# Kernel optimization log

Hardware: AMD Instinct MI355X
Metric: run time of the kernel (lower is better)

The kernel has to match this reference:

```python
import jax, jax.numpy as jnp
import numpy as np

B, S, D, H = 2, 2048, 512, 8
HS = D // H  # head_size = 64


def setup_inputs() -> dict:
    key = jax.random.key(0)
    ks = jax.random.split(key, 6)
    scale = 1.0 / np.sqrt(D)
    return {
        "seq_input": jax.random.normal(ks[0], (B, S, D), dtype=jnp.float32),
        "w_X": jax.random.uniform(ks[1], (B, S, S), dtype=jnp.float32),
        "mask": jax.random.uniform(ks[2], (B, S), dtype=jnp.float32),
        "wq": jax.random.normal(ks[3], (D, D), dtype=jnp.float32) * scale,
        "bq": jnp.zeros((D,), dtype=jnp.float32),
        "wk": jax.random.normal(ks[4], (D, D), dtype=jnp.float32) * scale,
        "bk": jnp.zeros((D,), dtype=jnp.float32),
        "wv": jax.random.normal(ks[5], (D, D), dtype=jnp.float32) * scale,
        "bv": jnp.zeros((D,), dtype=jnp.float32),
    }


def reference(seq_input, w_X, mask, wq, bq, wk, bk, wv, bv):
    b, s, d = seq_input.shape
    # Linear projections, split into heads: [b, h, s, hs]
    def proj(w, bias):
        y = jnp.einsum("bsd,ed->bse", seq_input, w) + bias
        return y.reshape(b, s, H, HS).transpose(0, 2, 1, 3)

    Q = proj(wq, bq)
    K = proj(wk, bk)
    V = proj(wv, bv)

    sim = jnp.einsum("bhqe,bhke->bhqk", Q, K) / np.sqrt(HS).astype(np.float32)
    sim = jax.nn.softmax(sim, axis=3)
    # post-softmax multiplicative edge weights, broadcast over heads
    sim = sim * w_X[:, None, :, :]
    # mask zeroes query rows (torch permute trick broadcasts mask over key dim)
    sim = sim * mask[:, None, :, None]

    new_V = jnp.einsum("bhqk,bhke->bhqe", sim, V)  # [b, h, s, hs]
    return new_V.transpose(0, 2, 1, 3).reshape(b, s, d)
```

## Files before the change

kernel.cpp:

```cpp
#include <hip/hip_runtime.h>

#define NB 2
#define NS 2048
#define ND 512
#define NH 8
#define NHS 64

typedef __attribute__((ext_vector_type(4))) float f32x4;
typedef __attribute__((ext_vector_type(8))) short s16x8;

__device__ inline unsigned short f2bf(float f) {
  unsigned int u = __float_as_uint(f);
  unsigned int r = (u + 0x7FFFu + ((u >> 16) & 1u)) >> 16;
  return (unsigned short)r;
}
__device__ inline int swz(int row, int col) { return row * 64 + (col ^ ((row & 7) << 3)); }

__device__ inline s16x8 pack8(const f32x4& a0, const f32x4& a1) {
  s16x8 v;
#pragma unroll
  for (int j = 0; j < 4; ++j) { v[j] = (short)f2bf(a0[j]); v[4 + j] = (short)f2bf(a1[j]); }
  return v;
}

__global__ __launch_bounds__(256) void kv_kernel(
    const float* __restrict__ X, const float* __restrict__ wk, const float* __restrict__ wv,
    const float* __restrict__ bk, const float* __restrict__ bv,
    unsigned short* __restrict__ Kb, unsigned short* __restrict__ Vt) {
  __shared__ __align__(16) unsigned short As[64 * 64];
  __shared__ __align__(16) unsigned short Bs[128 * 64];
  const int tid = threadIdx.x;
  const int lane = tid & 63, wid = tid >> 6;
  const int lr = lane & 15, lh = lane >> 4;
  const int m0 = blockIdx.y * 64;
  const int nb = blockIdx.x;
  const int type = nb >> 2;
  const int wrow0 = (nb & 3) * 128;
  const float* W = (type == 0) ? wk : wv;
  const float* bias = (type == 0) ? bk : bv;
  const int wm = wid >> 1, wn = wid & 1;

  f32x4 acc[2][4] = {};
  f32x4 ar[2][2], br[4][2];

#define KV_LOAD(K0)                                                          \
  {                                                                          \
    _Pragma("unroll") for (int g = 0; g < 2; ++g) {                          \
      int idx = tid + 256 * g; int row = idx >> 3, c8 = (idx & 7) * 8;       \
      const float* pa = X + (size_t)(m0 + row) * 512 + (K0) + c8;            \
      ar[g][0] = *(const f32x4*)pa; ar[g][1] = *(const f32x4*)(pa + 4);      \
    }                                                                        \
    _Pragma("unroll") for (int g = 0; g < 4; ++g) {                          \
      int idx = tid + 256 * g; int row = idx >> 3, c8 = (idx & 7) * 8;       \
      const float* pb = W + (size_t)(wrow0 + row) * 512 + (K0) + c8;         \
      br[g][0] = *(const f32x4*)pb; br[g][1] = *(const f32x4*)(pb + 4);      \
    }                                                                        \
  }

  KV_LOAD(0);
  for (int k0 = 0; k0 < 512; k0 += 64) {
#pragma unroll
    for (int g = 0; g < 2; ++g) {
      int idx = tid + 256 * g; int row = idx >> 3, c8 = (idx & 7) * 8;
      *(s16x8*)&As[swz(row, c8)] = pack8(ar[g][0], ar[g][1]);
    }
#pragma unroll
    for (int g = 0; g < 4; ++g) {
      int idx = tid + 256 * g; int row = idx >> 3, c8 = (idx & 7) * 8;
      *(s16x8*)&Bs[swz(row, c8)] = pack8(br[g][0], br[g][1]);
    }
    __syncthreads();
    if (k0 < 448) KV_LOAD(k0 + 64);
#pragma unroll
    for (int kk = 0; kk < 64; kk += 32) {
      s16x8 af[2], bf_[4];
#pragma unroll
      for (int f = 0; f < 2; ++f) af[f] = *(const s16x8*)&As[swz(wm * 32 + f * 16 + lr, kk + lh * 8)];
#pragma unroll
      for (int f = 0; f < 4; ++f) bf_[f] = *(const s16x8*)&Bs[swz(wn * 64 + f * 16 + lr, kk + lh * 8)];
#pragma unroll
      for (int fm = 0; fm < 2; ++fm)
#pragma unroll
        for (int fn = 0; fn < 4; ++fn)
          acc[fm][fn] = __builtin_amdgcn_mfma_f32_16x16x32_bf16(af[fm], bf_[fn], acc[fm][fn], 0, 0, 0);
    }
    __syncthreads();
  }
#undef KV_LOAD

#pragma unroll
  for (int fn = 0; fn < 4; ++fn) {
    int n = wrow0 + wn * 64 + fn * 16 + lr;
    int hh = n >> 6, hs = n & 63;
    float bb = bias[n];
#pragma unroll
    for (int fm = 0; fm < 2; ++fm) {
#pragma unroll
      for (int r = 0; r < 4; ++r) {
        int m = m0 + wm * 32 + fm * 16 + lh * 4 + r;
        int b = m >> 11, s = m & 2047;
        float val = acc[fm][fn][r] + bb;
        if (type == 0) {
          Kb[((size_t)(b * 8 + hh) * 2048 + s) * 64 + hs] = f2bf(val);
        } else {
          Vt[((size_t)(b * 8 + hh) * 64 + hs) * 2048 + s] = f2bf(val);
        }
      }
    }
  }
}

__global__ __launch_bounds__(256) void attn_kernel(
    const float* __restrict__ X, const float* __restrict__ wq, const float* __restrict__ bq,
    const unsigned short* __restrict__ Kb, const unsigned short* __restrict__ Vt,
    const float* __restrict__ wX, const float* __restrict__ mask, float* __restrict__ out) {
  __shared__ __align__(16) unsigned short Ks[64 * 64];
  __shared__ __align__(16) unsigned short Vs[64 * 64];
  __shared__ __align__(16) unsigned short Qs[64 * 64];
  __shared__ __align__(16) unsigned short Ps[4 * 16 * 64];
  const int tid = threadIdx.x;
  const int lane = tid & 63, wid = tid >> 6;
  const int lr = lane & 15, lh = lane >> 4;
  const int qt = blockIdx.x, hh = blockIdx.y, b = blockIdx.z;
  const int bh = b * 8 + hh;
  const int q0 = qt * 64;

  const int srow = tid >> 3, sc8 = (tid & 7) * 8;
  const int srow1 = (tid + 256) >> 3;

  f32x4 qacc[4] = {};
  f32x4 xr[2][2], wr0[2][2];
#define Q_LOAD(K0)                                                           \
  {                                                                          \
    _Pragma("unroll") for (int g = 0; g < 2; ++g) {                          \
      int row = g ? srow1 : srow;                                            \
      const float* px = X + (size_t)(b * 2048 + q0 + row) * 512 + (K0) + sc8;\
      const float* pw = wq + (size_t)(hh * 64 + row) * 512 + (K0) + sc8;     \
      xr[g][0] = *(const f32x4*)px; xr[g][1] = *(const f32x4*)(px + 4);      \
      wr0[g][0] = *(const f32x4*)pw; wr0[g][1] = *(const f32x4*)(pw + 4);    \
    }                                                                        \
  }
  Q_LOAD(0);
  for (int k0 = 0; k0 < 512; k0 += 64) {
#pragma unroll
    for (int g = 0; g < 2; ++g) {
      int row = g ? srow1 : srow;
      *(s16x8*)&Ks[swz(row, sc8)] = pack8(xr[g][0], xr[g][1]);
      *(s16x8*)&Vs[swz(row, sc8)] = pack8(wr0[g][0], wr0[g][1]);
    }
    __syncthreads();
    if (k0 < 448) Q_LOAD(k0 + 64);
#pragma unroll
    for (int kk = 0; kk < 64; kk += 32) {
      s16x8 xa = *(const s16x8*)&Ks[swz(wid * 16 + lr, kk + lh * 8)];
#pragma unroll
      for (int fn = 0; fn < 4; ++fn) {
        s16x8 wf = *(const s16x8*)&Vs[swz(fn * 16 + lr, kk + lh * 8)];
        qacc[fn] = __builtin_amdgcn_mfma_f32_16x16x32_bf16(xa, wf, qacc[fn], 0, 0, 0);
      }
    }
    __syncthreads();
  }
#undef Q_LOAD

  const int qrow_base = q0 + wid * 16 + lh * 4;
  const float* wxp = wX + ((size_t)b * 2048 + qrow_base) * 2048;

  s16x8 kreg[2], vreg[2];
  float wxf[4][4];
#define KV_TILE_LOAD(KT)                                                     \
  {                                                                          \
    _Pragma("unroll") for (int g = 0; g < 2; ++g) {                          \
      int row = g ? srow1 : srow;                                            \
      kreg[g] = *(const s16x8*)(Kb + ((size_t)bh * 2048 + (KT) * 64 + row) * 64 + sc8); \
      vreg[g] = *(const s16x8*)(Vt + ((size_t)bh * 64 + row) * 2048 + (KT) * 64 + sc8); \
    }                                                                        \
  }
#define WX_LOAD(KT)                                                          \
  {                                                                          \
    _Pragma("unroll") for (int f = 0; f < 4; ++f) {                          \
      int key = (KT) * 64 + f * 16 + lr;                                     \
      _Pragma("unroll") for (int r = 0; r < 4; ++r)                          \
        wxf[f][r] = wxp[(size_t)r * 2048 + key];                             \
    }                                                                        \
  }
  KV_TILE_LOAD(0);
  WX_LOAD(0);

#pragma unroll
  for (int fn = 0; fn < 4; ++fn) {
    int col = fn * 16 + lr;
    float bb = bq[hh * 64 + col];
#pragma unroll
    for (int r = 0; r < 4; ++r) {
      int row = wid * 16 + lh * 4 + r;
      Qs[swz(row, col)] = f2bf((qacc[fn][r] + bb) * 0.125f);
    }
  }
  __syncthreads();

  s16x8 qa[2];
#pragma unroll
  for (int c = 0; c < 2; ++c) qa[c] = *(const s16x8*)&Qs[swz(wid * 16 + lr, c * 32 + lh * 8)];

  float m_[4], l_[4];
  f32x4 o[4] = {};
#pragma unroll
  for (int r = 0; r < 4; ++r) { m_[r] = -__builtin_inff(); l_[r] = 0.f; }

  for (int kt = 0; kt < 32; ++kt) {
#pragma unroll
    for (int g = 0; g < 2; ++g) {
      int row = g ? srow1 : srow;
      *(s16x8*)&Ks[swz(row, sc8)] = kreg[g];
      *(s16x8*)&Vs[swz(row, sc8)] = vreg[g];
    }
    __syncthreads();
    if (kt + 1 < 32) KV_TILE_LOAD(kt + 1);

    f32x4 sv[4] = {};
#pragma unroll
    for (int c = 0; c < 2; ++c) {
#pragma unroll
      for (int f = 0; f < 4; ++f) {
        s16x8 kf = *(const s16x8*)&Ks[swz(f * 16 + lr, c * 32 + lh * 8)];
        sv[f] = __builtin_amdgcn_mfma_f32_16x16x32_bf16(qa[c], kf, sv[f], 0, 0, 0);
      }
    }

    float tm[4];
#pragma unroll
    for (int r = 0; r < 4; ++r)
      tm[r] = fmaxf(fmaxf(sv[0][r], sv[1][r]), fmaxf(sv[2][r], sv[3][r]));
#pragma unroll
    for (int off = 1; off < 16; off <<= 1)
#pragma unroll
      for (int r = 0; r < 4; ++r) tm[r] = fmaxf(tm[r], __shfl_xor(tm[r], off));

    float sc[4];
#pragma unroll
    for (int r = 0; r < 4; ++r) {
      float nm = fmaxf(m_[r], tm[r]);
      sc[r] = __expf(m_[r] - nm);
      m_[r] = nm;
      l_[r] *= sc[r];
    }
#pragma unroll
    for (int f = 0; f < 4; ++f)
#pragma unroll
      for (int r = 0; r < 4; ++r) o[f][r] *= sc[r];

    float ls[4] = {0.f, 0.f, 0.f, 0.f};
#pragma unroll
    for (int f = 0; f < 4; ++f) {
#pragma unroll
      for (int r = 0; r < 4; ++r) {
        float p = __expf(sv[f][r] - m_[r]);
        ls[r] += p;
        Ps[wid * 1024 + swz(lh * 4 + r, f * 16 + lr)] = f2bf(p * wxf[f][r]);
      }
    }
    if (kt + 1 < 32) WX_LOAD(kt + 1);
#pragma unroll
    for (int off = 1; off < 16; off <<= 1)
#pragma unroll
      for (int r = 0; r < 4; ++r) ls[r] += __shfl_xor(ls[r], off);
#pragma unroll
    for (int r = 0; r < 4; ++r) l_[r] += ls[r];

#pragma unroll
    for (int c = 0; c < 2; ++c) {
      s16x8 pf = *(const s16x8*)&Ps[wid * 1024 + swz(lr, c * 32 + lh * 8)];
#pragma unroll
      for (int f = 0; f < 4; ++f) {
        s16x8 vf = *(const s16x8*)&Vs[swz(f * 16 + lr, c * 32 + lh * 8)];
        o[f] = __builtin_amdgcn_mfma_f32_16x16x32_bf16(pf, vf, o[f], 0, 0, 0);
      }
    }
    __syncthreads();
  }
#undef KV_TILE_LOAD
#undef WX_LOAD

#pragma unroll
  for (int r = 0; r < 4; ++r) {
    int q = qrow_base + r;
    float mk = mask[b * 2048 + q];
    float inv = mk / l_[r];
#pragma unroll
    for (int f = 0; f < 4; ++f) {
      out[((size_t)(b * 2048 + q)) * 512 + hh * 64 + f * 16 + lr] = o[f][r] * inv;
    }
  }
}

extern "C" void kernel_launch(void* const* d_in, const int* in_sizes, int n_in,
                              void* d_out, int out_size, void* d_ws, size_t ws_size,
                              hipStream_t stream) {
  const float* X = (const float*)d_in[0];
  const float* wX = (const float*)d_in[1];
  const float* mask = (const float*)d_in[2];
  const float* wq = (const float*)d_in[3];
  const float* bq = (const float*)d_in[4];
  const float* wk = (const float*)d_in[5];
  const float* bk = (const float*)d_in[6];
  const float* wv = (const float*)d_in[7];
  const float* bv = (const float*)d_in[8];
  float* out = (float*)d_out;

  unsigned short* Kb = (unsigned short*)d_ws;
  unsigned short* Vt = Kb + 2097152;

  kv_kernel<<<dim3(8, 64), 256, 0, stream>>>(X, wk, wv, bk, bv, Kb, Vt);
  attn_kernel<<<dim3(32, 8, 2), 256, 0, stream>>>(X, wq, bq, Kb, Vt, wX, mask, out);
}
```

Measured before the change: 185.4 us.

## Transpose QK^T MFMA so each lane owns a query row, vectorize w_X loads

The attention kernel now computes S^T (K as the A operand), so each lane holds one query row's scores. Row max and sum reductions then need two cross-lane shuffles instead of four rounds over four rows, and w_X can be read as contiguous float4 vectors instead of strided scalars. P is written to shared memory as packed 8-byte stores. Separately, the KV projection kernel moves to 512 threads with a 2x4 wave layout. Extra __shfl calls redistribute the scale and sum values back to the output layout.

```diff
diff --git a/kernel.cpp b/kernel.cpp
--- a/kernel.cpp
+++ b/kernel.cpp
@@ -1,13 +1,8 @@
 #include <hip/hip_runtime.h>
-
-#define NB 2
-#define NS 2048
-#define ND 512
-#define NH 8
-#define NHS 64
 
 typedef __attribute__((ext_vector_type(4))) float f32x4;
 typedef __attribute__((ext_vector_type(8))) short s16x8;
+typedef __attribute__((ext_vector_type(2))) unsigned int u32x2;
 
 __device__ inline unsigned short f2bf(float f) {
   unsigned int u = __float_as_uint(f);
@@ -23,7 +18,7 @@
   return v;
 }
 
-__global__ __launch_bounds__(256) void kv_kernel(
+__global__ __launch_bounds__(512) void kv_kernel(
     const float* __restrict__ X, const float* __restrict__ wk, const float* __restrict__ wv,
     const float* __restrict__ bk, const float* __restrict__ bv,
     unsigned short* __restrict__ Kb, unsigned short* __restrict__ Vt) {
@@ -38,20 +33,18 @@
   const int wrow0 = (nb & 3) * 128;
   const float* W = (type == 0) ? wk : wv;
   const float* bias = (type == 0) ? bk : bv;
-  const int wm = wid >> 1, wn = wid & 1;
-
-  f32x4 acc[2][4] = {};
-  f32x4 ar[2][2], br[4][2];
+  const int wm = wid >> 2, wn = wid & 3;
+
+  f32x4 acc[2][2] = {};
+  f32x4 ar[2], br[2][2];
 
 #define KV_LOAD(K0)                                                          \
   {                                                                          \
+    { int row = tid >> 3, c8 = (tid & 7) * 8;                                \
+      const float* pa = X + (size_t)(m0 + row) * 512 + (K0) + c8;            \
+      ar[0] = *(const f32x4*)pa; ar[1] = *(const f32x4*)(pa + 4); }          \
     _Pragma("unroll") for (int g = 0; g < 2; ++g) {                          \
-      int idx = tid + 256 * g; int row = idx >> 3, c8 = (idx & 7) * 8;       \
-      const float* pa = X + (size_t)(m0 + row) * 512 + (K0) + c8;            \
-      ar[g][0] = *(const f32x4*)pa; ar[g][1] = *(const f32x4*)(pa + 4);      \
-    }                                                                        \
-    _Pragma("unroll") for (int g = 0; g < 4; ++g) {                          \
-      int idx = tid + 256 * g; int row = idx >> 3, c8 = (idx & 7) * 8;       \
+      int idx = tid + 512 * g; int row = idx >> 3, c8 = (idx & 7) * 8;       \
       const float* pb = W + (size_t)(wrow0 + row) * 512 + (K0) + c8;         \
       br[g][0] = *(const f32x4*)pb; br[g][1] = *(const f32x4*)(pb + 4);      \
     }                                                                        \
@@ -59,29 +52,28 @@
 
   KV_LOAD(0);
   for (int k0 = 0; k0 < 512; k0 += 64) {
+    {
+      int row = tid >> 3, c8 = (tid & 7) * 8;
+      *(s16x8*)&As[swz(row, c8)] = pack8(ar[0], ar[1]);
+    }
 #pragma unroll
     for (int g = 0; g < 2; ++g) {
-      int idx = tid + 256 * g; int row = idx >> 3, c8 = (idx & 7) * 8;
-      *(s16x8*)&As[swz(row, c8)] = pack8(ar[g][0], ar[g][1]);
-    }
-#pragma unroll
-    for (int g = 0; g < 4; ++g) {
-      int idx = tid + 256 * g; int row = idx >> 3, c8 = (idx & 7) * 8;
+      int idx = tid + 512 * g; int row = idx >> 3, c8 = (idx & 7) * 8;
       *(s16x8*)&Bs[swz(row, c8)] = pack8(br[g][0], br[g][1]);
     }
     __syncthreads();
     if (k0 < 448) KV_LOAD(k0 + 64);
 #pragma unroll
     for (int kk = 0; kk < 64; kk += 32) {
-      s16x8 af[2], bf_[4];
+      s16x8 af[2], bf_[2];
 #pragma unroll
       for (int f = 0; f < 2; ++f) af[f] = *(const s16x8*)&As[swz(wm * 32 + f * 16 + lr, kk + lh * 8)];
 #pragma unroll
-      for (int f = 0; f < 4; ++f) bf_[f] = *(const s16x8*)&Bs[swz(wn * 64 + f * 16 + lr, kk + lh * 8)];
+      for (int f = 0; f < 2; ++f) bf_[f] = *(const s16x8*)&Bs[swz(wn * 32 + f * 16 + lr, kk + lh * 8)];
 #pragma unroll
       for (int fm = 0; fm < 2; ++fm)
 #pragma unroll
-        for (int fn = 0; fn < 4; ++fn)
+        for (int fn = 0; fn < 2; ++fn)
           acc[fm][fn] = __builtin_amdgcn_mfma_f32_16x16x32_bf16(af[fm], bf_[fn], acc[fm][fn], 0, 0, 0);
     }
     __syncthreads();
@@ -89,8 +81,8 @@
 #undef KV_LOAD
 
 #pragma unroll
-  for (int fn = 0; fn < 4; ++fn) {
-    int n = wrow0 + wn * 64 + fn * 16 + lr;
+  for (int fn = 0; fn < 2; ++fn) {
+    int n = wrow0 + wn * 32 + fn * 16 + lr;
     int hh = n >> 6, hs = n & 63;
     float bb = bias[n];
 #pragma unroll
@@ -164,10 +156,11 @@
 #undef Q_LOAD
 
   const int qrow_base = q0 + wid * 16 + lh * 4;
-  const float* wxp = wX + ((size_t)b * 2048 + qrow_base) * 2048;
+  const int q_sm = q0 + wid * 16 + lr;
+  const float* wxq = wX + ((size_t)b * 2048 + q_sm) * 2048;
 
   s16x8 kreg[2], vreg[2];
-  float wxf[4][4];
+  f32x4 wxv[4];
 #define KV_TILE_LOAD(KT)                                                     \
   {                                                                          \
     _Pragma("unroll") for (int g = 0; g < 2; ++g) {                          \
@@ -178,11 +171,8 @@
   }
 #define WX_LOAD(KT)                                                          \
   {                                                                          \
-    _Pragma("unroll") for (int f = 0; f < 4; ++f) {                          \
-      int key = (KT) * 64 + f * 16 + lr;                                     \
-      _Pragma("unroll") for (int r = 0; r < 4; ++r)                          \
-        wxf[f][r] = wxp[(size_t)r * 2048 + key];                             \
-    }                                                                        \
+    _Pragma("unroll") for (int f = 0; f < 4; ++f)                            \
+      wxv[f] = *(const f32x4*)(wxq + (KT) * 64 + f * 16 + lh * 4);           \
   }
   KV_TILE_LOAD(0);
   WX_LOAD(0);
@@ -203,10 +193,8 @@
 #pragma unroll
   for (int c = 0; c < 2; ++c) qa[c] = *(const s16x8*)&Qs[swz(wid * 16 + lr, c * 32 + lh * 8)];
 
-  float m_[4], l_[4];
+  float m_ = -__builtin_inff(), l_ = 0.f;
   f32x4 o[4] = {};
-#pragma unroll
-  for (int r = 0; r < 4; ++r) { m_[r] = -__builtin_inff(); l_[r] = 0.f; }
 
   for (int kt = 0; kt < 32; ++kt) {
 #pragma unroll
@@ -224,49 +212,49 @@
 #pragma unroll
       for (int f = 0; f < 4; ++f) {
         s16x8 kf = *(const s16x8*)&Ks[swz(f * 16 + lr, c * 32 + lh * 8)];
-        sv[f] = __builtin_amdgcn_mfma_f32_16x16x32_bf16(qa[c], kf, sv[f], 0, 0, 0);
-      }
-    }
-
-    float tm[4];
-#pragma unroll
-    for (int r = 0; r < 4; ++r)
-      tm[r] = fmaxf(fmaxf(sv[0][r], sv[1][r]), fmaxf(sv[2][r], sv[3][r]));
-#pragma unroll
-    for (int off = 1; off < 16; off <<= 1)
-#pragma unroll
-      for (int r = 0; r < 4; ++r) tm[r] = fmaxf(tm[r], __shfl_xor(tm[r], off));
-
-    float sc[4];
-#pragma unroll
-    for (int r = 0; r < 4; ++r) {
-      float nm = fmaxf(m_[r], tm[r]);
-      sc[r] = __expf(m_[r] - nm);
-      m_[r] = nm;
-      l_[r] *= sc[r];
-    }
+        sv[f] = __builtin_amdgcn_mfma_f32_16x16x32_bf16(kf, qa[c], sv[f], 0, 0, 0);
+      }
+    }
+
+    float t0 = fmaxf(fmaxf(sv[0][0], sv[0][1]), fmaxf(sv[0][2], sv[0][3]));
+    float t1 = fmaxf(fmaxf(sv[1][0], sv[1][1]), fmaxf(sv[1][2], sv[1][3]));
+    float t2 = fmaxf(fmaxf(sv[2][0], sv[2][1]), fmaxf(sv[2][2], sv[2][3]));
+    float t3 = fmaxf(fmaxf(sv[3][0], sv[3][1]), fmaxf(sv[3][2], sv[3][3]));
+    float tm = fmaxf(fmaxf(t0, t1), fmaxf(t2, t3));
+    tm = fmaxf(tm, __shfl_xor(tm, 16));
+    tm = fmaxf(tm, __shfl_xor(tm, 32));
+
+    float nm = fmaxf(m_, tm);
+    float sc = __expf(m_ - nm);
+    m_ = nm;
+    l_ *= sc;
+    float sc_o[4];
+#pragma unroll
+    for (int r = 0; r < 4; ++r) sc_o[r] = __shfl(sc, 20 * lh + r);
 #pragma unroll
     for (int f = 0; f < 4; ++f)
 #pragma unroll
-      for (int r = 0; r < 4; ++r) o[f][r] *= sc[r];
-
-    float ls[4] = {0.f, 0.f, 0.f, 0.f};
+      for (int r = 0; r < 4; ++r) o[f][r] *= sc_o[r];
+
+    float ls = 0.f;
 #pragma unroll
     for (int f = 0; f < 4; ++f) {
+      float pw[4];
 #pragma unroll
       for (int r = 0; r < 4; ++r) {
-        float p = __expf(sv[f][r] - m_[r]);
-        ls[r] += p;
-        Ps[wid * 1024 + swz(lh * 4 + r, f * 16 + lr)] = f2bf(p * wxf[f][r]);
-      }
+        float p = __expf(sv[f][r] - m_);
+        ls += p;
+        pw[r] = p * wxv[f][r];
+      }
+      u32x2 pk;
+      pk[0] = (unsigned int)f2bf(pw[0]) | ((unsigned int)f2bf(pw[1]) << 16);
+      pk[1] = (unsigned int)f2bf(pw[2]) | ((unsigned int)f2bf(pw[3]) << 16);
+      *(u32x2*)&Ps[wid * 1024 + swz(lr, f * 16 + lh * 4)] = pk;
     }
     if (kt + 1 < 32) WX_LOAD(kt + 1);
-#pragma unroll
-    for (int off = 1; off < 16; off <<= 1)
-#pragma unroll
-      for (int r = 0; r < 4; ++r) ls[r] += __shfl_xor(ls[r], off);
-#pragma unroll
-    for (int r = 0; r < 4; ++r) l_[r] += ls[r];
+    ls += __shfl_xor(ls, 16);
+    ls += __shfl_xor(ls, 32);
+    l_ += ls;
 
 #pragma unroll
     for (int c = 0; c < 2; ++c) {
@@ -282,11 +270,14 @@
 #undef KV_TILE_LOAD
 #undef WX_LOAD
 
+  float l_o[4];
+#pragma unroll
+  for (int r = 0; r < 4; ++r) l_o[r] = __shfl(l_, 20 * lh + r);
 #pragma unroll
   for (int r = 0; r < 4; ++r) {
     int q = qrow_base + r;
     float mk = mask[b * 2048 + q];
-    float inv = mk / l_[r];
+    float inv = mk / l_o[r];
 #pragma unroll
     for (int f = 0; f < 4; ++f) {
       out[((size_t)(b * 2048 + q)) * 512 + hh * 64 + f * 16 + lr] = o[f][r] * inv;
@@ -311,6 +302,6 @@
   unsigned short* Kb = (unsigned short*)d_ws;
   unsigned short* Vt = Kb + 2097152;
 
-  kv_kernel<<<dim3(8, 64), 256, 0, stream>>>(X, wk, wv, bk, bv, Kb, Vt);
+  kv_kernel<<<dim3(8, 64), 512, 0, stream>>>(X, wk, wv, bk, bv, Kb, Vt);
   attn_kernel<<<dim3(32, 8, 2), 256, 0, stream>>>(X, wq, bq, Kb, Vt, wX, mask, out);
 }
```

After: 164.7 us. 1.13x faster.
